# Optimization experiments

Hardware: AMD Instinct MI355X
Metric: run time of the kernel (lower is better)

## Reference

```python
import jax, jax.numpy as jnp
import numpy as np

D_DYN, D_STAT, H, T, B = 3, 3, 256, 365, 1024


def setup_inputs() -> dict:
    key = jax.random.key(0)
    ks = jax.random.split(key, 8)
    C = D_DYN + H
    s = lambda k, shape: jax.random.normal(k, shape, dtype=jnp.float32) * 0.05
    return {
        "x_dyn": jax.random.normal(ks[0], (B, T, D_DYN), dtype=jnp.float32),
        "x_stat": jax.random.normal(ks[1], (B, D_STAT), dtype=jnp.float32),
        "w_i": s(ks[2], (D_STAT, H)), "b_i": jnp.zeros((H,), jnp.float32),
        "w_f": s(ks[3], (C, H)), "b_f": jnp.zeros((H,), jnp.float32),
        "w_g": s(ks[4], (C, H)), "b_g": jnp.zeros((H,), jnp.float32),
        "w_o": s(ks[5], (C, H)), "b_o": jnp.zeros((H,), jnp.float32),
        "w_head": s(ks[6], (H, 1)), "b_head": jnp.zeros((1,), jnp.float32),
    }


def reference(x_dyn, x_stat, w_i, b_i, w_f, b_f, w_g, b_g, w_o, b_o, w_head, b_head):
    # Static input gate (EA-LSTM): i depends only on static features.
    i = jax.nn.sigmoid(x_stat @ w_i + b_i)  # (B, H)

    # Merge the three gate linears into one (C, 3H) matmul per step and
    # split the concat [x_t, h] into x- and h-parts (equivalent to torch.cat).
    W = jnp.concatenate([w_f, w_g, w_o], axis=1)  # (C, 3H)
    Wx, Wh = W[:D_DYN], W[D_DYN:]                 # (D,3H), (H,3H)
    b = jnp.concatenate([b_f, b_g, b_o])          # (3H,)

    def step(carry, x_t):
        h, c = carry
        z = x_t @ Wx + h @ Wh + b                 # (B, 3H)
        f = jax.nn.sigmoid(z[:, :H])
        g = jnp.tanh(z[:, H:2 * H])
        o = jax.nn.sigmoid(z[:, 2 * H:])
        c = f * c + i * g
        h = o * jnp.tanh(c)
        return (h, c), None

    h0 = jnp.zeros((x_dyn.shape[0], H), x_dyn.dtype)
    c0 = jnp.zeros((x_dyn.shape[0], H), x_dyn.dtype)
    (h, _), _ = jax.lax.scan(step, (h0, c0), jnp.swapaxes(x_dyn, 0, 1))
    # Dropout is identity in eval mode.
    return h @ w_head + b_head  # (B, 1)
```

## Files before the change

kernel.cpp:

```cpp
#include <hip/hip_runtime.h>
#include <hip/hip_bf16.h>

#define T_STEPS 365
#define XLEN    (T_STEPS * 3)
#define H_SZ    256
#define ROWS    16
#define NW      8
#define CPW     32

#define SF1     (-1.4426950408889634f)
#define SF2     (-2.8853900817779268f)

typedef __attribute__((ext_vector_type(8))) short bf16x8;
typedef __attribute__((ext_vector_type(4))) short bf16x4;
typedef __attribute__((ext_vector_type(4))) float f32x4;

__device__ __forceinline__ float fast_sigmoid(float x) {
    return __builtin_amdgcn_rcpf(1.0f + __builtin_amdgcn_exp2f(-1.44269504f * x));
}
__device__ __forceinline__ unsigned short f2bf(float x) {
    __hip_bfloat16 b = __float2bfloat16(x);
    return *reinterpret_cast<unsigned short*>(&b);
}
__device__ __forceinline__ float bf2f(unsigned short v) {
    return __uint_as_float(((unsigned)v) << 16);
}
__device__ __forceinline__ bf16x8 expand4(bf16x4 v) {
    bf16x8 r = (bf16x8)0;
    r[0] = v[0]; r[1] = v[1]; r[2] = v[2]; r[3] = v[3];
    return r;
}

__global__ void __launch_bounds__(256)
xstage(const float* __restrict__ x_dyn, unsigned short* __restrict__ xg)
{
    const int rb = blockIdx.x * ROWS;
    for (int idx = threadIdx.x; idx < T_STEPS * ROWS; idx += 256) {
        const int t = idx % T_STEPS, r = idx / T_STEPS;
        const float* s = x_dyn + (size_t)(rb + r) * XLEN + t * 3;
        bf16x4 pk;
        pk[0] = (short)f2bf(s[0]); pk[1] = (short)f2bf(s[1]);
        pk[2] = (short)f2bf(s[2]); pk[3] = (short)0x3F80;
        *(bf16x4*)&xg[((size_t)blockIdx.x * T_STEPS + t) * 64 + r * 4] = pk;
    }
}

__global__ void __launch_bounds__(512, 2)
ealstm_fused(const unsigned short* __restrict__ xg, const float* __restrict__ x_stat,
             const float* __restrict__ w_i, const float* __restrict__ b_i,
             const float* __restrict__ w_f, const float* __restrict__ b_f,
             const float* __restrict__ w_g, const float* __restrict__ b_g,
             const float* __restrict__ w_o, const float* __restrict__ b_o,
             const float* __restrict__ w_head, const float* __restrict__ b_head,
             float* __restrict__ out)
{
    const int tid   = threadIdx.x;
    const int lane  = tid & 63;
    const int wv    = tid >> 6;
    const int m     = lane & 15;
    const int l16   = lane >> 4;
    const int rb    = blockIdx.x * ROWS;
    const int wbase = wv * CPW;

    __shared__ unsigned short wo_lds[4 * 8 * 256 * 8];
    __shared__ unsigned short hbuf[2][4096];
    __shared__ float          red[NW][ROWS];

    for (int idx = tid; idx < 4 * 8 * 8 * 256; idx += 512) {
        const int c    = idx & 255;
        const int e    = (idx >> 8) & 7;
        const int kt   = (idx >> 11) & 7;
        const int l16g = idx >> 14;
        wo_lds[((l16g * 8 + kt) * 256 + c) * 8 + e] =
            f2bf(SF1 * w_o[(3 + kt * 32 + l16g * 8 + e) * H_SZ + c]);
    }
    for (int idx = tid; idx < 2048; idx += 512) ((unsigned int*)hbuf[0])[idx] = 0u;

    const float* wsrc[3] = {w_f, w_g, w_o};
    const float* bsrc[3] = {b_f, b_g, b_o};
    const float  gsf[3]  = {SF1, SF2, SF1};

    bf16x8 wA[8][2][2];
    bf16x4 wX[2][3];
#pragma unroll
    for (int ct = 0; ct < 2; ++ct) {
        const int c = wbase + ct * 16 + m;
#pragma unroll
        for (int g = 0; g < 2; ++g)
#pragma unroll
            for (int kt = 0; kt < 8; ++kt) {
                bf16x8 a;
#pragma unroll
                for (int e = 0; e < 8; ++e)
                    a[e] = (short)f2bf(gsf[g] * wsrc[g][(3 + kt * 32 + l16 * 8 + e) * H_SZ + c]);
                wA[kt][ct][g] = a;
            }
#pragma unroll
        for (int g = 0; g < 3; ++g) {
            bf16x4 ax = (bf16x4)0;
            if (l16 == 0) {
                ax[0] = (short)f2bf(gsf[g] * wsrc[g][0 * H_SZ + c]);
                ax[1] = (short)f2bf(gsf[g] * wsrc[g][1 * H_SZ + c]);
                ax[2] = (short)f2bf(gsf[g] * wsrc[g][2 * H_SZ + c]);
                ax[3] = (short)f2bf(gsf[g] * bsrc[g][c]);
            }
            wX[ct][g] = ax;
        }
    }

    float iv[2][4], cst[2][4];
    {
        const float xs0 = x_stat[(rb + m) * 3 + 0];
        const float xs1 = x_stat[(rb + m) * 3 + 1];
        const float xs2 = x_stat[(rb + m) * 3 + 2];
#pragma unroll
        for (int ct = 0; ct < 2; ++ct)
#pragma unroll
            for (int q = 0; q < 4; ++q) {
                const int c = wbase + ct * 16 + l16 * 4 + q;
                iv[ct][q] = fast_sigmoid(b_i[c] + xs0 * w_i[c] + xs1 * w_i[H_SZ + c]
                                                + xs2 * w_i[2 * H_SZ + c]);
                cst[ct][q] = 0.0f;
            }
    }

    int woff[2];
#pragma unroll
    for (int ct = 0; ct < 2; ++ct) {
        const int c0 = wbase + ct * 16 + l16 * 4;
        woff[ct] = ((c0 >> 5) * 64 + m + 16 * ((c0 & 31) >> 3)) * 8 + (c0 & 7);
    }

    const unsigned short* xrow   = xg + (size_t)blockIdx.x * T_STEPS * 64 + m * 4;
    const bf16x8*         wobase = (const bf16x8*)&wo_lds[((l16 * 8) * 256 + wbase + m) * 8];

    __syncthreads();

    for (int t = 0; t < T_STEPS; ++t) {
        const int cur = t & 1;
        const bf16x8* hp = (const bf16x8*)hbuf[cur] + lane;
        unsigned short* hw = hbuf[cur ^ 1];

        bf16x8 xf = (bf16x8)0;
        {
            unsigned long long xv = *(const unsigned long long*)&xrow[(size_t)t * 64];
            if (l16 != 0) xv = 0ULL;
            union { unsigned long long u; bf16x4 v; } X; X.u = xv;
            xf[0] = X.v[0]; xf[1] = X.v[1]; xf[2] = X.v[2]; xf[3] = X.v[3];
        }
        bf16x8 hb[8];
#pragma unroll
        for (int kt = 0; kt < 8; ++kt) hb[kt] = hp[kt * 64];

        f32x4 acc[2][3];
        const f32x4 z4 = {0.f, 0.f, 0.f, 0.f};

#pragma unroll
        for (int g = 0; g < 3; ++g)
            acc[0][g] = __builtin_amdgcn_mfma_f32_16x16x32_bf16(
                expand4(wX[0][g]), xf, z4, 0, 0, 0);
#pragma unroll
        for (int kt = 0; kt < 8; ++kt) {
            const bf16x8 wo0 = wobase[kt * 256];
            acc[0][0] = __builtin_amdgcn_mfma_f32_16x16x32_bf16(wA[kt][0][0], hb[kt], acc[0][0], 0, 0, 0);
            acc[0][1] = __builtin_amdgcn_mfma_f32_16x16x32_bf16(wA[kt][0][1], hb[kt], acc[0][1], 0, 0, 0);
            acc[0][2] = __builtin_amdgcn_mfma_f32_16x16x32_bf16(wo0,          hb[kt], acc[0][2], 0, 0, 0);
        }
        {
            bf16x4 pk;
#pragma unroll
            for (int q = 0; q < 4; ++q) {
                const float fq = __builtin_amdgcn_rcpf(1.0f + __builtin_amdgcn_exp2f(acc[0][0][q]));
                const float gq = 2.0f * __builtin_amdgcn_rcpf(1.0f + __builtin_amdgcn_exp2f(acc[0][1][q])) - 1.0f;
                const float oq = __builtin_amdgcn_rcpf(1.0f + __builtin_amdgcn_exp2f(acc[0][2][q]));
                const float cq = fq * cst[0][q] + iv[0][q] * gq;
                cst[0][q] = cq;
                const float th = 2.0f * __builtin_amdgcn_rcpf(1.0f + __builtin_amdgcn_exp2f(SF2 * cq)) - 1.0f;
                pk[q] = (short)f2bf(oq * th);
            }
            *(bf16x4*)&hw[woff[0]] = pk;
        }

#pragma unroll
        for (int g = 0; g < 3; ++g)
            acc[1][g] = __builtin_amdgcn_mfma_f32_16x16x32_bf16(
                expand4(wX[1][g]), xf, z4, 0, 0, 0);
#pragma unroll
        for (int kt = 0; kt < 8; ++kt) {
            const bf16x8 wo1 = wobase[kt * 256 + 16];
            acc[1][0] = __builtin_amdgcn_mfma_f32_16x16x32_bf16(wA[kt][1][0], hb[kt], acc[1][0], 0, 0, 0);
            acc[1][1] = __builtin_amdgcn_mfma_f32_16x16x32_bf16(wA[kt][1][1], hb[kt], acc[1][1], 0, 0, 0);
            acc[1][2] = __builtin_amdgcn_mfma_f32_16x16x32_bf16(wo1,          hb[kt], acc[1][2], 0, 0, 0);
        }
        {
            bf16x4 pk;
#pragma unroll
            for (int q = 0; q < 4; ++q) {
                const float fq = __builtin_amdgcn_rcpf(1.0f + __builtin_amdgcn_exp2f(acc[1][0][q]));
                const float gq = 2.0f * __builtin_amdgcn_rcpf(1.0f + __builtin_amdgcn_exp2f(acc[1][1][q])) - 1.0f;
                const float oq = __builtin_amdgcn_rcpf(1.0f + __builtin_amdgcn_exp2f(acc[1][2][q]));
                const float cq = fq * cst[1][q] + iv[1][q] * gq;
                cst[1][q] = cq;
                const float th = 2.0f * __builtin_amdgcn_rcpf(1.0f + __builtin_amdgcn_exp2f(SF2 * cq)) - 1.0f;
                pk[q] = (short)f2bf(oq * th);
            }
            *(bf16x4*)&hw[woff[1]] = pk;
        }
        __syncthreads();
    }

    float p = 0.0f;
    const unsigned short* hf = hbuf[1];
#pragma unroll
    for (int ct = 0; ct < 2; ++ct) {
        const int c0 = wbase + ct * 16 + l16 * 4;
        const f32x4 wh = *(const f32x4*)&w_head[c0];
        const bf16x4 hv = *(const bf16x4*)&hf[woff[ct]];
#pragma unroll
        for (int q = 0; q < 4; ++q) p += bf2f((unsigned short)hv[q]) * wh[q];
    }
    p += __shfl_xor(p, 16);
    p += __shfl_xor(p, 32);
    if (lane < 16) red[wv][m] = p;
    __syncthreads();
    if (tid < ROWS) {
        float s = b_head[0];
#pragma unroll
        for (int w = 0; w < NW; ++w) s += red[w][tid];
        out[rb + tid] = s;
    }
}

extern "C" void kernel_launch(void* const* d_in, const int* in_sizes, int n_in,
                              void* d_out, int out_size, void* d_ws, size_t ws_size,
                              hipStream_t stream)
{
    const float* x_dyn  = (const float*)d_in[0];
    const float* x_stat = (const float*)d_in[1];
    const float* w_i    = (const float*)d_in[2];
    const float* b_i    = (const float*)d_in[3];
    const float* w_f    = (const float*)d_in[4];
    const float* b_f    = (const float*)d_in[5];
    const float* w_g    = (const float*)d_in[6];
    const float* b_g    = (const float*)d_in[7];
    const float* w_o    = (const float*)d_in[8];
    const float* b_o    = (const float*)d_in[9];
    const float* w_head = (const float*)d_in[10];
    const float* b_head = (const float*)d_in[11];

    unsigned short* xg = (unsigned short*)d_ws;

    xstage<<<dim3(64), dim3(256), 0, stream>>>(x_dyn, xg);
    ealstm_fused<<<dim3(64), dim3(512), 0, stream>>>(
        xg, x_stat, w_i, b_i, w_f, b_f, w_g, b_g, w_o, b_o,
        w_head, b_head, (float*)d_out);
}
```

Baseline: 569.1 us.

## Skew wave groups so gate math overlaps the other half's MFMAs

```diff
diff --git a/kernel.cpp b/kernel.cpp
--- a/kernel.cpp
+++ b/kernel.cpp
@@ -29,6 +29,22 @@
     bf16x8 r = (bf16x8)0;
     r[0] = v[0]; r[1] = v[1]; r[2] = v[2]; r[3] = v[3];
     return r;
+}
+__device__ __forceinline__ bf16x4 do_gates(const f32x4 zf, const f32x4 zg,
+                                           const f32x4 zo, const float iv[4],
+                                           float cst[4]) {
+    bf16x4 pk;
+#pragma unroll
+    for (int q = 0; q < 4; ++q) {
+        const float fq = __builtin_amdgcn_rcpf(1.0f + __builtin_amdgcn_exp2f(zf[q]));
+        const float gq = 2.0f * __builtin_amdgcn_rcpf(1.0f + __builtin_amdgcn_exp2f(zg[q])) - 1.0f;
+        const float oq = __builtin_amdgcn_rcpf(1.0f + __builtin_amdgcn_exp2f(zo[q]));
+        const float cq = fq * cst[q] + iv[q] * gq;
+        cst[q] = cq;
+        const float th = 2.0f * __builtin_amdgcn_rcpf(1.0f + __builtin_amdgcn_exp2f(SF2 * cq)) - 1.0f;
+        pk[q] = (short)f2bf(oq * th);
+    }
+    return pk;
 }
 
 __global__ void __launch_bounds__(256)
@@ -61,6 +77,7 @@
     const int l16   = lane >> 4;
     const int rb    = blockIdx.x * ROWS;
     const int wbase = wv * CPW;
+    const bool grpA = (wv < 4);
 
     __shared__ unsigned short wo_lds[4 * 8 * 256 * 8];
     __shared__ unsigned short hbuf[2][4096];
@@ -134,80 +151,117 @@
     const unsigned short* xrow   = xg + (size_t)blockIdx.x * T_STEPS * 64 + m * 4;
     const bf16x8*         wobase = (const bf16x8*)&wo_lds[((l16 * 8) * 256 + wbase + m) * 8];
 
+    f32x4 accB[2][3];
+
     __syncthreads();
 
     for (int t = 0; t < T_STEPS; ++t) {
-        const int cur = t & 1;
-        const bf16x8* hp = (const bf16x8*)hbuf[cur] + lane;
-        unsigned short* hw = hbuf[cur ^ 1];
-
-        bf16x8 xf = (bf16x8)0;
-        {
-            unsigned long long xv = *(const unsigned long long*)&xrow[(size_t)t * 64];
-            if (l16 != 0) xv = 0ULL;
-            union { unsigned long long u; bf16x4 v; } X; X.u = xv;
-            xf[0] = X.v[0]; xf[1] = X.v[1]; xf[2] = X.v[2]; xf[3] = X.v[3];
-        }
-        bf16x8 hb[8];
-#pragma unroll
-        for (int kt = 0; kt < 8; ++kt) hb[kt] = hp[kt * 64];
-
-        f32x4 acc[2][3];
-        const f32x4 z4 = {0.f, 0.f, 0.f, 0.f};
-
-#pragma unroll
-        for (int g = 0; g < 3; ++g)
-            acc[0][g] = __builtin_amdgcn_mfma_f32_16x16x32_bf16(
-                expand4(wX[0][g]), xf, z4, 0, 0, 0);
-#pragma unroll
-        for (int kt = 0; kt < 8; ++kt) {
-            const bf16x8 wo0 = wobase[kt * 256];
-            acc[0][0] = __builtin_amdgcn_mfma_f32_16x16x32_bf16(wA[kt][0][0], hb[kt], acc[0][0], 0, 0, 0);
-            acc[0][1] = __builtin_amdgcn_mfma_f32_16x16x32_bf16(wA[kt][0][1], hb[kt], acc[0][1], 0, 0, 0);
-            acc[0][2] = __builtin_amdgcn_mfma_f32_16x16x32_bf16(wo0,          hb[kt], acc[0][2], 0, 0, 0);
-        }
-        {
-            bf16x4 pk;
-#pragma unroll
-            for (int q = 0; q < 4; ++q) {
-                const float fq = __builtin_amdgcn_rcpf(1.0f + __builtin_amdgcn_exp2f(acc[0][0][q]));
-                const float gq = 2.0f * __builtin_amdgcn_rcpf(1.0f + __builtin_amdgcn_exp2f(acc[0][1][q])) - 1.0f;
-                const float oq = __builtin_amdgcn_rcpf(1.0f + __builtin_amdgcn_exp2f(acc[0][2][q]));
-                const float cq = fq * cst[0][q] + iv[0][q] * gq;
-                cst[0][q] = cq;
-                const float th = 2.0f * __builtin_amdgcn_rcpf(1.0f + __builtin_amdgcn_exp2f(SF2 * cq)) - 1.0f;
-                pk[q] = (short)f2bf(oq * th);
-            }
-            *(bf16x4*)&hw[woff[0]] = pk;
-        }
-
-#pragma unroll
-        for (int g = 0; g < 3; ++g)
-            acc[1][g] = __builtin_amdgcn_mfma_f32_16x16x32_bf16(
-                expand4(wX[1][g]), xf, z4, 0, 0, 0);
-#pragma unroll
-        for (int kt = 0; kt < 8; ++kt) {
-            const bf16x8 wo1 = wobase[kt * 256 + 16];
-            acc[1][0] = __builtin_amdgcn_mfma_f32_16x16x32_bf16(wA[kt][1][0], hb[kt], acc[1][0], 0, 0, 0);
-            acc[1][1] = __builtin_amdgcn_mfma_f32_16x16x32_bf16(wA[kt][1][1], hb[kt], acc[1][1], 0, 0, 0);
-            acc[1][2] = __builtin_amdgcn_mfma_f32_16x16x32_bf16(wo1,          hb[kt], acc[1][2], 0, 0, 0);
-        }
-        {
-            bf16x4 pk;
-#pragma unroll
-            for (int q = 0; q < 4; ++q) {
-                const float fq = __builtin_amdgcn_rcpf(1.0f + __builtin_amdgcn_exp2f(acc[1][0][q]));
-                const float gq = 2.0f * __builtin_amdgcn_rcpf(1.0f + __builtin_amdgcn_exp2f(acc[1][1][q])) - 1.0f;
-                const float oq = __builtin_amdgcn_rcpf(1.0f + __builtin_amdgcn_exp2f(acc[1][2][q]));
-                const float cq = fq * cst[1][q] + iv[1][q] * gq;
-                cst[1][q] = cq;
-                const float th = 2.0f * __builtin_amdgcn_rcpf(1.0f + __builtin_amdgcn_exp2f(SF2 * cq)) - 1.0f;
-                pk[q] = (short)f2bf(oq * th);
-            }
-            *(bf16x4*)&hw[woff[1]] = pk;
+        const bf16x8* hp = (const bf16x8*)hbuf[t & 1] + lane;
+        unsigned short* hwW = hbuf[(t + 1) & 1];
+        unsigned short* hwP = hbuf[t & 1];
+
+        f32x4 accA[2][3];
+        bf16x8 xfA = (bf16x8)0;
+
+        if (grpA) {
+            {
+                unsigned long long xv = *(const unsigned long long*)&xrow[(size_t)t * 64];
+                if (l16 != 0) xv = 0ULL;
+                union { unsigned long long u; bf16x4 v; } X; X.u = xv;
+                xfA[0] = X.v[0]; xfA[1] = X.v[1]; xfA[2] = X.v[2]; xfA[3] = X.v[3];
+            }
+            const f32x4 z4 = {0.f, 0.f, 0.f, 0.f};
+            bf16x8 hb0 = hp[0];
+#pragma unroll
+            for (int ct = 0; ct < 2; ++ct) {
+                accA[ct][0] = __builtin_amdgcn_mfma_f32_16x16x32_bf16(wA[0][ct][0], hb0, z4, 0, 0, 0);
+                accA[ct][1] = __builtin_amdgcn_mfma_f32_16x16x32_bf16(wA[0][ct][1], hb0, z4, 0, 0, 0);
+                accA[ct][2] = __builtin_amdgcn_mfma_f32_16x16x32_bf16(wobase[ct * 16], hb0, z4, 0, 0, 0);
+            }
+#pragma unroll
+            for (int kt = 1; kt < 4; ++kt) {
+                const bf16x8 b = hp[kt * 64];
+#pragma unroll
+                for (int ct = 0; ct < 2; ++ct) {
+                    accA[ct][0] = __builtin_amdgcn_mfma_f32_16x16x32_bf16(wA[kt][ct][0], b, accA[ct][0], 0, 0, 0);
+                    accA[ct][1] = __builtin_amdgcn_mfma_f32_16x16x32_bf16(wA[kt][ct][1], b, accA[ct][1], 0, 0, 0);
+                    accA[ct][2] = __builtin_amdgcn_mfma_f32_16x16x32_bf16(wobase[kt * 256 + ct * 16], b, accA[ct][2], 0, 0, 0);
+                }
+            }
+        } else {
+            if (t > 0) {
+                const bf16x4 pk0 = do_gates(accB[0][0], accB[0][1], accB[0][2], iv[0], cst[0]);
+                *(bf16x4*)&hwP[woff[0]] = pk0;
+                const bf16x4 pk1 = do_gates(accB[1][0], accB[1][1], accB[1][2], iv[1], cst[1]);
+                *(bf16x4*)&hwP[woff[1]] = pk1;
+            }
         }
         __syncthreads();
-    }
+
+        if (grpA) {
+#pragma unroll
+            for (int kt = 4; kt < 8; ++kt) {
+                const bf16x8 b = hp[kt * 64];
+#pragma unroll
+                for (int ct = 0; ct < 2; ++ct) {
+                    accA[ct][0] = __builtin_amdgcn_mfma_f32_16x16x32_bf16(wA[kt][ct][0], b, accA[ct][0], 0, 0, 0);
+                    accA[ct][1] = __builtin_amdgcn_mfma_f32_16x16x32_bf16(wA[kt][ct][1], b, accA[ct][1], 0, 0, 0);
+                    accA[ct][2] = __builtin_amdgcn_mfma_f32_16x16x32_bf16(wobase[kt * 256 + ct * 16], b, accA[ct][2], 0, 0, 0);
+                }
+            }
+#pragma unroll
+            for (int ct = 0; ct < 2; ++ct)
+#pragma unroll
+                for (int g = 0; g < 3; ++g)
+                    accA[ct][g] = __builtin_amdgcn_mfma_f32_16x16x32_bf16(
+                        expand4(wX[ct][g]), xfA, accA[ct][g], 0, 0, 0);
+            const bf16x4 pk0 = do_gates(accA[0][0], accA[0][1], accA[0][2], iv[0], cst[0]);
+            *(bf16x4*)&hwW[woff[0]] = pk0;
+            const bf16x4 pk1 = do_gates(accA[1][0], accA[1][1], accA[1][2], iv[1], cst[1]);
+            *(bf16x4*)&hwW[woff[1]] = pk1;
+        } else {
+            bf16x8 xfB = (bf16x8)0;
+            {
+                unsigned long long xv = *(const unsigned long long*)&xrow[(size_t)t * 64];
+                if (l16 != 0) xv = 0ULL;
+                union { unsigned long long u; bf16x4 v; } X; X.u = xv;
+                xfB[0] = X.v[0]; xfB[1] = X.v[1]; xfB[2] = X.v[2]; xfB[3] = X.v[3];
+            }
+            const f32x4 z4 = {0.f, 0.f, 0.f, 0.f};
+            bf16x8 hb0 = hp[0];
+#pragma unroll
+            for (int ct = 0; ct < 2; ++ct) {
+                accB[ct][0] = __builtin_amdgcn_mfma_f32_16x16x32_bf16(wA[0][ct][0], hb0, z4, 0, 0, 0);
+                accB[ct][1] = __builtin_amdgcn_mfma_f32_16x16x32_bf16(wA[0][ct][1], hb0, z4, 0, 0, 0);
+                accB[ct][2] = __builtin_amdgcn_mfma_f32_16x16x32_bf16(wobase[ct * 16], hb0, z4, 0, 0, 0);
+            }
+#pragma unroll
+            for (int kt = 1; kt < 8; ++kt) {
+                const bf16x8 b = hp[kt * 64];
+#pragma unroll
+                for (int ct = 0; ct < 2; ++ct) {
+                    accB[ct][0] = __builtin_amdgcn_mfma_f32_16x16x32_bf16(wA[kt][ct][0], b, accB[ct][0], 0, 0, 0);
+                    accB[ct][1] = __builtin_amdgcn_mfma_f32_16x16x32_bf16(wA[kt][ct][1], b, accB[ct][1], 0, 0, 0);
+                    accB[ct][2] = __builtin_amdgcn_mfma_f32_16x16x32_bf16(wobase[kt * 256 + ct * 16], b, accB[ct][2], 0, 0, 0);
+                }
+            }
+#pragma unroll
+            for (int ct = 0; ct < 2; ++ct)
+#pragma unroll
+                for (int g = 0; g < 3; ++g)
+                    accB[ct][g] = __builtin_amdgcn_mfma_f32_16x16x32_bf16(
+                        expand4(wX[ct][g]), xfB, accB[ct][g], 0, 0, 0);
+        }
+        __syncthreads();
+    }
+
+    if (!grpA) {
+        const bf16x4 pk0 = do_gates(accB[0][0], accB[0][1], accB[0][2], iv[0], cst[0]);
+        *(bf16x4*)&hbuf[1][woff[0]] = pk0;
+        const bf16x4 pk1 = do_gates(accB[1][0], accB[1][1], accB[1][2], iv[1], cst[1]);
+        *(bf16x4*)&hbuf[1][woff[1]] = pk1;
+    }
+    __syncthreads();
 
     float p = 0.0f;
     const unsigned short* hf = hbuf[1];
```

New measurement: 609.2 us. 1.07x slower.

## Interleave both column-tile MFMA chains and merge gate reciprocals algebraically

Applied to the files above, without the earlier changes.

```diff
diff --git a/kernel.cpp b/kernel.cpp
--- a/kernel.cpp
+++ b/kernel.cpp
@@ -81,7 +81,7 @@
     const float  gsf[3]  = {SF1, SF2, SF1};
 
     bf16x8 wA[8][2][2];
-    bf16x4 wX[2][3];
+    bf16x8 wXe[2][3];
 #pragma unroll
     for (int ct = 0; ct < 2; ++ct) {
         const int c = wbase + ct * 16 + m;
@@ -104,7 +104,7 @@
                 ax[2] = (short)f2bf(gsf[g] * wsrc[g][2 * H_SZ + c]);
                 ax[3] = (short)f2bf(gsf[g] * bsrc[g][c]);
             }
-            wX[ct][g] = ax;
+            wXe[ct][g] = expand4(ax);
         }
     }
 
@@ -151,60 +151,54 @@
         bf16x8 hb[8];
 #pragma unroll
         for (int kt = 0; kt < 8; ++kt) hb[kt] = hp[kt * 64];
+        bf16x8 wor[8][2];
+#pragma unroll
+        for (int kt = 0; kt < 8; ++kt) {
+            wor[kt][0] = wobase[kt * 256];
+            wor[kt][1] = wobase[kt * 256 + 16];
+        }
 
         f32x4 acc[2][3];
-        const f32x4 z4 = {0.f, 0.f, 0.f, 0.f};
-
-#pragma unroll
-        for (int g = 0; g < 3; ++g)
-            acc[0][g] = __builtin_amdgcn_mfma_f32_16x16x32_bf16(
-                expand4(wX[0][g]), xf, z4, 0, 0, 0);
+        {
+            const f32x4 z4 = {0.f, 0.f, 0.f, 0.f};
+#pragma unroll
+            for (int ct = 0; ct < 2; ++ct)
+#pragma unroll
+                for (int g = 0; g < 3; ++g)
+                    acc[ct][g] = __builtin_amdgcn_mfma_f32_16x16x32_bf16(
+                        wXe[ct][g], xf, z4, 0, 0, 0);
+        }
+
 #pragma unroll
         for (int kt = 0; kt < 8; ++kt) {
-            const bf16x8 wo0 = wobase[kt * 256];
             acc[0][0] = __builtin_amdgcn_mfma_f32_16x16x32_bf16(wA[kt][0][0], hb[kt], acc[0][0], 0, 0, 0);
             acc[0][1] = __builtin_amdgcn_mfma_f32_16x16x32_bf16(wA[kt][0][1], hb[kt], acc[0][1], 0, 0, 0);
-            acc[0][2] = __builtin_amdgcn_mfma_f32_16x16x32_bf16(wo0,          hb[kt], acc[0][2], 0, 0, 0);
-        }
-        {
-            bf16x4 pk;
-#pragma unroll
-            for (int q = 0; q < 4; ++q) {
-                const float fq = __builtin_amdgcn_rcpf(1.0f + __builtin_amdgcn_exp2f(acc[0][0][q]));
-                const float gq = 2.0f * __builtin_amdgcn_rcpf(1.0f + __builtin_amdgcn_exp2f(acc[0][1][q])) - 1.0f;
-                const float oq = __builtin_amdgcn_rcpf(1.0f + __builtin_amdgcn_exp2f(acc[0][2][q]));
-                const float cq = fq * cst[0][q] + iv[0][q] * gq;
-                cst[0][q] = cq;
-                const float th = 2.0f * __builtin_amdgcn_rcpf(1.0f + __builtin_amdgcn_exp2f(SF2 * cq)) - 1.0f;
-                pk[q] = (short)f2bf(oq * th);
-            }
-            *(bf16x4*)&hw[woff[0]] = pk;
-        }
-
-#pragma unroll
-        for (int g = 0; g < 3; ++g)
-            acc[1][g] = __builtin_amdgcn_mfma_f32_16x16x32_bf16(
-                expand4(wX[1][g]), xf, z4, 0, 0, 0);
-#pragma unroll
-        for (int kt = 0; kt < 8; ++kt) {
-            const bf16x8 wo1 = wobase[kt * 256 + 16];
+            acc[0][2] = __builtin_amdgcn_mfma_f32_16x16x32_bf16(wor[kt][0],   hb[kt], acc[0][2], 0, 0, 0);
             acc[1][0] = __builtin_amdgcn_mfma_f32_16x16x32_bf16(wA[kt][1][0], hb[kt], acc[1][0], 0, 0, 0);
             acc[1][1] = __builtin_amdgcn_mfma_f32_16x16x32_bf16(wA[kt][1][1], hb[kt], acc[1][1], 0, 0, 0);
-            acc[1][2] = __builtin_amdgcn_mfma_f32_16x16x32_bf16(wo1,          hb[kt], acc[1][2], 0, 0, 0);
-        }
-        {
+            acc[1][2] = __builtin_amdgcn_mfma_f32_16x16x32_bf16(wor[kt][1],   hb[kt], acc[1][2], 0, 0, 0);
+        }
+
+#pragma unroll
+        for (int ct = 0; ct < 2; ++ct) {
             bf16x4 pk;
 #pragma unroll
             for (int q = 0; q < 4; ++q) {
-                const float fq = __builtin_amdgcn_rcpf(1.0f + __builtin_amdgcn_exp2f(acc[1][0][q]));
-                const float gq = 2.0f * __builtin_amdgcn_rcpf(1.0f + __builtin_amdgcn_exp2f(acc[1][1][q])) - 1.0f;
-                const float oq = __builtin_amdgcn_rcpf(1.0f + __builtin_amdgcn_exp2f(acc[1][2][q]));
-                const float cq = fq * cst[1][q] + iv[1][q] * gq;
-                cst[1][q] = cq;
-                const float th = 2.0f * __builtin_amdgcn_rcpf(1.0f + __builtin_amdgcn_exp2f(SF2 * cq)) - 1.0f;
-                pk[q] = (short)f2bf(oq * th);
-            }
-            *(bf16x4*)&hw[woff[1]] = pk;
+                const float Ef = __builtin_amdgcn_exp2f(acc[ct][0][q]);
+                const float Eg = __builtin_amdgcn_exp2f(acc[ct][1][q]);
+                const float Eo = __builtin_amdgcn_exp2f(acc[ct][2][q]);
+                const float u  = 1.0f + Eg;
+                const float v  = 1.0f + Ef;
+                const float t2 = iv[ct][q] * (2.0f - u);
+                const float cq = (cst[ct][q] * u + t2 * v) *
+                                 __builtin_amdgcn_rcpf(u * v);
+                cst[ct][q] = cq;
+                const float Ec = __builtin_amdgcn_exp2f(SF2 * cq);
+                const float hq = (1.0f - Ec) *
+                                 __builtin_amdgcn_rcpf((1.0f + Eo) * (1.0f + Ec));
+                pk[q] = (short)f2bf(hq);
+            }
+            *(bf16x4*)&hw[woff[ct]] = pk;
         }
         __syncthreads();
     }
```

New measurement: 578.1 us. Within noise of the previous version (+1.6%).
